# Performance work log

Measured on AMD Instinct MI355X. Metric: run time of the kernel, lower is better.

## Reference

```python
import jax, jax.numpy as jnp
import numpy as np

B, N, F_IN, H = 16, 1024, 64, 256
NEG = -9e15
ALPHA = 0.2  # LeakyReLU slope


def _leaky(x):
    return jnp.where(x >= 0, x, ALPHA * x)


def setup_inputs() -> dict:
    key = jax.random.key(0)
    ks = jax.random.split(key, 12)
    s = lambda k, shape, fan: jax.random.normal(k, shape, jnp.float32) / np.sqrt(fan)
    node_features = jax.random.normal(ks[0], (B, N, F_IN), jnp.float32)
    adj_matrix = jax.random.randint(ks[1], (B, N, N), 0, 2).astype(jnp.float32)
    return {
        "node_features": node_features,
        "adj_matrix": adj_matrix,
        "emb_W": s(ks[2], (F_IN, H), F_IN),
        "emb_b": jnp.zeros((H,), jnp.float32),
        "W0": s(ks[3], (H, H), H),
        "a1_0": s(ks[4], (H,), H),
        "a2_0": s(ks[5], (H,), H),
        "W1": s(ks[6], (H, H), H),
        "a1_1": s(ks[7], (H,), H),
        "a2_1": s(ks[8], (H,), H),
        "gp_W1": s(ks[9], (H, H), H),
        "gp_b1": jnp.zeros((H,), jnp.float32),
        "gp_W2": s(ks[10], (H, H), H),
        "gp_b2": jnp.zeros((H,), jnp.float32),
    }


def _gat_layer(x, mask, W, a1, a2):
    # x: [B,N,H]; mask: [B,N,N] bool. Equivalent to original concat trick:
    # a([h_i || h_j]) = h_i @ a1 + h_j @ a2 with a.weight split in halves.
    h = jnp.einsum('bnf,fo->bno', x, W)              # [B,N,H]
    s1 = jnp.einsum('bnh,h->bn', h, a1)              # [B,N]
    s2 = jnp.einsum('bnh,h->bn', h, a2)              # [B,N]
    e = _leaky(s1[:, :, None] + s2[:, None, :])      # [B,N,N]
    att = jax.nn.softmax(jnp.where(mask, e, NEG), axis=2)
    # dropout p=0.2 is identity in eval mode
    return jnp.einsum('bij,bjh->bih', att, h)        # [B,N,H]


def reference(node_features, adj_matrix, emb_W, emb_b,
              W0, a1_0, a2_0, W1, a1_1, a2_1,
              gp_W1, gp_b1, gp_W2, gp_b2):
    mask = adj_matrix > 0
    x = jnp.einsum('bnf,fh->bnh', node_features, emb_W) + emb_b
    x = jax.nn.relu(_gat_layer(x, mask, W0, a1_0, a2_0))
    x = jax.nn.relu(_gat_layer(x, mask, W1, a1_1, a2_1))
    g = jnp.mean(x, axis=1) + jnp.max(x, axis=1)     # [B,H]
    g = jax.nn.relu(g @ gp_W1 + gp_b1) @ gp_W2 + gp_b2
    return x, g
```

## Files before the change

### kernel.cpp

```cpp
#include <hip/hip_runtime.h>
#include <hip/hip_bf16.h>

#define B 16
#define N 1024
#define F_IN 64
#define H 256
#define ALPHA 0.2f
#define LOG2E 1.44269504f

typedef __attribute__((ext_vector_type(8))) _Float16 half8;
typedef __attribute__((ext_vector_type(4))) _Float16 half4;
typedef __attribute__((ext_vector_type(4))) float floatx4;
typedef __attribute__((ext_vector_type(16))) float floatx16;

#if __has_builtin(__builtin_amdgcn_exp2f)
#define EXP2F(x) __builtin_amdgcn_exp2f(x)
#else
#define EXP2F(x) exp2f(x)
#endif

__device__ __forceinline__ floatx4 mfma_f16(half8 a, half8 b, floatx4 c) {
    return __builtin_amdgcn_mfma_f32_16x16x32_f16(a, b, c, 0, 0, 0);
}
__device__ __forceinline__ floatx16 mfma32_f16(half8 a, half8 b, floatx16 c) {
    return __builtin_amdgcn_mfma_f32_32x32x16_f16(a, b, c, 0, 0, 0);
}

__global__ __launch_bounds__(256) void k_prep(const float* __restrict__ embW,
                                              const float* __restrict__ W0, const float* __restrict__ W1,
                                              const float* __restrict__ a10, const float* __restrict__ a20,
                                              const float* __restrict__ a11, const float* __restrict__ a21,
                                              _Float16* __restrict__ wBf,
                                              _Float16* __restrict__ embf,
                                              float* __restrict__ wa1, float* __restrict__ wa2,
                                              int* __restrict__ cnt) {
    __shared__ float lds[256 * 17];
    const int blk = blockIdx.x;
    const int t = threadIdx.x;
    const int lane = t & 63;

    if (blk == 34) {
        if (t < B) cnt[t] = 0;
        for (int s = t; s < 2048; s += 256) {
            const int ln = s & 63, ct2 = s >> 6;
            const int ct = ct2 >> 1, ks2 = ct2 & 1;
            const int q = ln >> 4, lw = ln & 15;
            half8 bf;
#pragma unroll
            for (int e = 0; e < 8; e++)
                bf[e] = (_Float16)embW[(ks2 * 32 + q * 8 + e) * H + ct * 16 + lw];
            *(half8*)(embf + (size_t)s * 8) = bf;
        }
        return;
    }
    if (blk >= 32) {
        const int l = blk - 32;
        const float* W = l ? W1 : W0;
        const float* a1 = l ? a11 : a10;
        const float* a2 = l ? a21 : a20;
        float* a1s = lds;
        float* a2s = lds + 256;
        a1s[t] = a1[t]; a2s[t] = a2[t];
        __syncthreads();
        float v1 = 0.f, v2 = 0.f;
        for (int c = 0; c < H; c += 4) {
            float4 w = *(const float4*)&W[t * H + c];
            v1 += w.x * a1s[c] + w.y * a1s[c + 1] + w.z * a1s[c + 2] + w.w * a1s[c + 3];
            v2 += w.x * a2s[c] + w.y * a2s[c + 1] + w.z * a2s[c + 2] + w.w * a2s[c + 3];
        }
        wa1[l * H + t] = v1;
        wa2[l * H + t] = v2;
        return;
    }
    const int l = blk >> 4, ct = blk & 15;
    const float* W = l ? W1 : W0;
#pragma unroll
    for (int rep = 0; rep < 16; rep++) {
        int idx = rep * 256 + t;
        int k = idx >> 4, cl = idx & 15;
        lds[k * 17 + cl] = W[k * H + ct * 16 + cl];
    }
    __syncthreads();
    const int w = t >> 6;
    const int l15 = lane & 15, quad = lane >> 4;
#pragma unroll
    for (int e = 0; e < 2; e++) {
        const int ks = w * 2 + e;
        half8 bf;
#pragma unroll
        for (int jj = 0; jj < 8; jj++)
            bf[jj] = (_Float16)lds[(ks * 32 + quad * 8 + jj) * 17 + l15];
        *(half8*)(wBf + (size_t)(((l * 16 + ct) * 8 + ks) * 64 + lane) * 8) = bf;
    }
}

#define XS(it, ks) ((((it) * 8 + (ks))) * 520)
__global__ __launch_bounds__(256, 4) void k_mix(const float* __restrict__ adj,
                                                const float* __restrict__ nf,
                                                const _Float16* __restrict__ embf,
                                                const float* __restrict__ embB,
                                                const _Float16* __restrict__ wBf,
                                                const float* __restrict__ wa1, const float* __restrict__ wa2,
                                                unsigned* __restrict__ mask32,
                                                _Float16* __restrict__ hB,
                                                float* __restrict__ s1, float* __restrict__ s2) {
    __shared__ __align__(16) _Float16 sm[8320];
    const int blk = blockIdx.x;
    const int t = threadIdx.x;
    const int lane = t & 63;

    if (blk & 1) {
        const int id = blk >> 1;
        const int wv = id * 4 + (t >> 6);
#pragma unroll 2
        for (int task = wv; task < B * N * 4; task += 4096) {
            const float4 v = *(const float4*)(adj + (size_t)task * 256 + lane * 4);
            unsigned long long b0 = __ballot(v.x > 0.f);
            unsigned long long b1 = __ballot(v.y > 0.f);
            unsigned long long b2 = __ballot(v.z > 0.f);
            unsigned long long b3 = __ballot(v.w > 0.f);
            if (lane < 8) {
                unsigned w0 = (unsigned)((b0 >> (8 * lane)) & 0xff)
                            | ((unsigned)((b1 >> (8 * lane)) & 0xff) << 8)
                            | ((unsigned)((b2 >> (8 * lane)) & 0xff) << 16)
                            | ((unsigned)((b3 >> (8 * lane)) & 0xff) << 24);
                const int jg = task & 3, row = task >> 2;
                mask32[(size_t)row * 32 + jg * 8 + lane] = w0;
            }
        }
        return;
    }

    const int lin = blk >> 1;
    const int rc = lin >> 1, chalf = lin & 1;
    const int row0 = rc * 32;
    const int w = t >> 6;
    const int l15 = lane & 15, quad = lane >> 4;

    {
        half8 anf[2][2];
#pragma unroll
        for (int it = 0; it < 2; it++)
#pragma unroll
            for (int ks2 = 0; ks2 < 2; ks2++) {
                const float* src = nf + (size_t)(row0 + it * 16 + l15) * F_IN + ks2 * 32 + quad * 8;
                float4 f0 = *(const float4*)(src);
                float4 f1 = *(const float4*)(src + 4);
                half8 a;
                a[0] = (_Float16)f0.x; a[1] = (_Float16)f0.y;
                a[2] = (_Float16)f0.z; a[3] = (_Float16)f0.w;
                a[4] = (_Float16)f1.x; a[5] = (_Float16)f1.y;
                a[6] = (_Float16)f1.z; a[7] = (_Float16)f1.w;
                anf[it][ks2] = a;
            }
#pragma unroll
        for (int ctl = 0; ctl < 4; ctl++) {
            const int ct = w * 4 + ctl;
            half8 be0 = *(const half8*)(embf + (size_t)((ct * 2 + 0) * 64 + lane) * 8);
            half8 be1 = *(const half8*)(embf + (size_t)((ct * 2 + 1) * 64 + lane) * 8);
            const int col = ct * 16 + l15;
            const float bias = embB[col];
            const int ks = col >> 5, qd = (col >> 3) & 3, e = col & 7;
#pragma unroll
            for (int it = 0; it < 2; it++) {
                floatx4 xa = {0.f, 0.f, 0.f, 0.f};
                xa = mfma_f16(anf[it][0], be0, xa);
                xa = mfma_f16(anf[it][1], be1, xa);
#pragma unroll
                for (int r = 0; r < 4; r++)
                    sm[XS(it, ks) + (qd * 16 + quad * 4 + r) * 8 + e] = (_Float16)(xa[r] + bias);
            }
        }
    }
    __syncthreads();

    const int ct0 = chalf * 8 + 2 * w;
    const _Float16* pB0 = wBf + (size_t)((ct0 * 8) * 64 + lane) * 8;
    const _Float16* pB1 = wBf + (size_t)(((ct0 + 1) * 8) * 64 + lane) * 8;

    floatx4 acc[2][2];
    floatx4 z = {0.f, 0.f, 0.f, 0.f};
    acc[0][0] = z; acc[0][1] = z; acc[1][0] = z; acc[1][1] = z;
    float sp1a = 0.f, sp2a = 0.f, sp1b = 0.f, sp2b = 0.f;

    half8 B0 = *(const half8*)(pB0);
    half8 B1 = *(const half8*)(pB1);

#pragma unroll
    for (int ks = 0; ks < 8; ks++) {
        half8 nB0 = B0, nB1 = B1;
        if (ks < 7) {
            const int o = (ks + 1) * 512;
            nB0 = *(const half8*)(pB0 + o);
            nB1 = *(const half8*)(pB1 + o);
        }
        half8 A0 = *(const half8*)(sm + XS(0, ks) + lane * 8);
        half8 A1 = *(const half8*)(sm + XS(1, ks) + lane * 8);
        acc[0][0] = mfma_f16(A0, B0, acc[0][0]);
        acc[0][1] = mfma_f16(A0, B1, acc[0][1]);
        acc[1][0] = mfma_f16(A1, B0, acc[1][0]);
        acc[1][1] = mfma_f16(A1, B1, acc[1][1]);
        if (chalf == 0 && w == 0) {
            float4 w1a = *(const float4*)(wa1 + ks * 32 + quad * 8);
            float4 w1b = *(const float4*)(wa1 + ks * 32 + quad * 8 + 4);
            float4 w2a = *(const float4*)(wa2 + ks * 32 + quad * 8);
            float4 w2b = *(const float4*)(wa2 + ks * 32 + quad * 8 + 4);
            float wv1[8] = {w1a.x, w1a.y, w1a.z, w1a.w, w1b.x, w1b.y, w1b.z, w1b.w};
            float wv2[8] = {w2a.x, w2a.y, w2a.z, w2a.w, w2b.x, w2b.y, w2b.z, w2b.w};
#pragma unroll
            for (int j = 0; j < 8; j++) {
                float xa = (float)A0[j];
                float xb = (float)A1[j];
                sp1a += xa * wv1[j]; sp2a += xa * wv2[j];
                sp1b += xb * wv1[j]; sp2b += xb * wv2[j];
            }
        }
        B0 = nB0; B1 = nB1;
    }

    __syncthreads();
    _Float16* trc = sm;
#pragma unroll
    for (int rg = 0; rg < 2; rg++) {
#pragma unroll
        for (int n2 = 0; n2 < 2; n2++) {
            const int c_l = (2 * w + n2) * 16 + l15;
            half4 hv;
            hv[0] = (_Float16)acc[rg][n2][0];
            hv[1] = (_Float16)acc[rg][n2][1];
            hv[2] = (_Float16)acc[rg][n2][2];
            hv[3] = (_Float16)acc[rg][n2][3];
            *(half4*)(trc + c_l * 40 + rg * 16 + quad * 4) = hv;
        }
    }
    __syncthreads();
    {
        const int bb = row0 >> 10, jtb = (row0 >> 5) & 31;
#pragma unroll
        for (int rep = 0; rep < 2; rep++) {
            int slot = rep * 256 + t;
            int l = slot & 63, frag = slot >> 6;
            int k4 = frag >> 1, ks = frag & 1;
            int c_l = k4 * 32 + (l & 31);
            int roff = ks * 16 + (l >> 5) * 8;
            half8 hv = *(const half8*)(trc + c_l * 40 + roff);
            _Float16* dst = hB + ((size_t)((bb * 8 + chalf * 4 + k4) * 32 + jtb) * 2 + ks) * 512 + l * 8;
            *(half8*)dst = hv;
        }
    }
    if (chalf == 0 && w == 0) {
        sp1a += __shfl_xor(sp1a, 16); sp1a += __shfl_xor(sp1a, 32);
        sp2a += __shfl_xor(sp2a, 16); sp2a += __shfl_xor(sp2a, 32);
        sp1b += __shfl_xor(sp1b, 16); sp1b += __shfl_xor(sp1b, 32);
        sp2b += __shfl_xor(sp2b, 16); sp2b += __shfl_xor(sp2b, 32);
        if (quad == 0) {
            s1[row0 + l15] = sp1a; s2[row0 + l15] = sp2a;
            s1[row0 + 16 + l15] = sp1b; s2[row0 + 16 + l15] = sp2b;
        }
    }
}

__global__ __launch_bounds__(256, 4) void k_gemm(const _Float16* __restrict__ xf,
                                                 const _Float16* __restrict__ wBf,
                                                 const float* __restrict__ wa1, const float* __restrict__ wa2,
                                                 _Float16* __restrict__ hB,
                                                 float* __restrict__ s1, float* __restrict__ s2) {
    __shared__ __align__(16) _Float16 sm[8320];
    const int lin = blockIdx.x;
    const int rc = lin >> 1, chalf = lin & 1;
    const int row0 = rc * 32;
    const int t = threadIdx.x;
    const int lane = t & 63, w = t >> 6;
    const int l15 = lane & 15, quad = lane >> 4;

#pragma unroll
    for (int pass = 0; pass < 4; pass++) {
        int idx = pass * 256 + t;
        int row_l = idx >> 5, k8 = idx & 31;
        half8 v = *(const half8*)(xf + (size_t)(row0 + row_l) * H + k8 * 8);
        int it = row_l >> 4, lf = row_l & 15, ks = k8 >> 2, qd = k8 & 3;
        *(half8*)(sm + XS(it, ks) + (qd * 16 + lf) * 8) = v;
    }
    __syncthreads();

    const int ct0 = chalf * 8 + 2 * w;
    const _Float16* pB0 = wBf + (size_t)((ct0 * 8) * 64 + lane) * 8;
    const _Float16* pB1 = wBf + (size_t)(((ct0 + 1) * 8) * 64 + lane) * 8;

    floatx4 acc[2][2];
    floatx4 z = {0.f, 0.f, 0.f, 0.f};
    acc[0][0] = z; acc[0][1] = z; acc[1][0] = z; acc[1][1] = z;
    float sp1a = 0.f, sp2a = 0.f, sp1b = 0.f, sp2b = 0.f;

    half8 B0 = *(const half8*)(pB0);
    half8 B1 = *(const half8*)(pB1);

#pragma unroll
    for (int ks = 0; ks < 8; ks++) {
        half8 nB0 = B0, nB1 = B1;
        if (ks < 7) {
            const int o = (ks + 1) * 512;
            nB0 = *(const half8*)(pB0 + o);
            nB1 = *(const half8*)(pB1 + o);
        }
        half8 A0 = *(const half8*)(sm + XS(0, ks) + lane * 8);
        half8 A1 = *(const half8*)(sm + XS(1, ks) + lane * 8);
        acc[0][0] = mfma_f16(A0, B0, acc[0][0]);
        acc[0][1] = mfma_f16(A0, B1, acc[0][1]);
        acc[1][0] = mfma_f16(A1, B0, acc[1][0]);
        acc[1][1] = mfma_f16(A1, B1, acc[1][1]);
        if (chalf == 0 && w == 0) {
            float4 w1a = *(const float4*)(wa1 + ks * 32 + quad * 8);
            float4 w1b = *(const float4*)(wa1 + ks * 32 + quad * 8 + 4);
            float4 w2a = *(const float4*)(wa2 + ks * 32 + quad * 8);
            float4 w2b = *(const float4*)(wa2 + ks * 32 + quad * 8 + 4);
            float wv1[8] = {w1a.x, w1a.y, w1a.z, w1a.w, w1b.x, w1b.y, w1b.z, w1b.w};
            float wv2[8] = {w2a.x, w2a.y, w2a.z, w2a.w, w2b.x, w2b.y, w2b.z, w2b.w};
#pragma unroll
            for (int j = 0; j < 8; j++) {
                float xa = (float)A0[j];
                float xb = (float)A1[j];
                sp1a += xa * wv1[j]; sp2a += xa * wv2[j];
                sp1b += xb * wv1[j]; sp2b += xb * wv2[j];
            }
        }
        B0 = nB0; B1 = nB1;
    }

    __syncthreads();
    _Float16* trc = sm;
#pragma unroll
    for (int rg = 0; rg < 2; rg++) {
#pragma unroll
        for (int n2 = 0; n2 < 2; n2++) {
            const int c_l = (2 * w + n2) * 16 + l15;
            half4 hv;
            hv[0] = (_Float16)acc[rg][n2][0];
            hv[1] = (_Float16)acc[rg][n2][1];
            hv[2] = (_Float16)acc[rg][n2][2];
            hv[3] = (_Float16)acc[rg][n2][3];
            *(half4*)(trc + c_l * 40 + rg * 16 + quad * 4) = hv;
        }
    }
    __syncthreads();
    {
        const int bb = row0 >> 10, jtb = (row0 >> 5) & 31;
#pragma unroll
        for (int rep = 0; rep < 2; rep++) {
            int slot = rep * 256 + t;
            int l = slot & 63, frag = slot >> 6;
            int k4 = frag >> 1, ks = frag & 1;
            int c_l = k4 * 32 + (l & 31);
            int roff = ks * 16 + (l >> 5) * 8;
            half8 hv = *(const half8*)(trc + c_l * 40 + roff);
            _Float16* dst = hB + ((size_t)((bb * 8 + chalf * 4 + k4) * 32 + jtb) * 2 + ks) * 512 + l * 8;
            *(half8*)dst = hv;
        }
    }
    if (chalf == 0 && w == 0) {
        sp1a += __shfl_xor(sp1a, 16); sp1a += __shfl_xor(sp1a, 32);
        sp2a += __shfl_xor(sp2a, 16); sp2a += __shfl_xor(sp2a, 32);
        sp1b += __shfl_xor(sp1b, 16); sp1b += __shfl_xor(sp1b, 32);
        sp2b += __shfl_xor(sp2b, 16); sp2b += __shfl_xor(sp2b, 32);
        if (quad == 0) {
            s1[row0 + l15] = sp1a; s2[row0 + l15] = sp2a;
            s1[row0 + 16 + l15] = sp1b; s2[row0 + 16 + l15] = sp2b;
        }
    }
}

template <int LAST>
__global__ __launch_bounds__(256, 1) void k_gat(const _Float16* __restrict__ hB,
                                                const float* __restrict__ s1g,
                                                const float* __restrict__ s2g,
                                                const unsigned* __restrict__ mask32,
                                                float* __restrict__ outf,
                                                _Float16* __restrict__ oxf,
                                                float* __restrict__ psum, float* __restrict__ pmax,
                                                const float* __restrict__ gpW1, const float* __restrict__ gpb1,
                                                const float* __restrict__ gpW2, const float* __restrict__ gpb2,
                                                float* __restrict__ gout, int* __restrict__ cnt) {
    __shared__ float s2s[N];
    __shared__ unsigned msk[128][33];
    __shared__ float wmax[4];
    __shared__ float red1[4][128];
    __shared__ float red2[4][128];
    __shared__ int lastf;
    const int lin = blockIdx.x;
    const int xcd = lin & 7, sl = lin >> 3;
    const int b = xcd * 2 + (sl & 1);
    const int chunk = (sl >> 1) & 7;
    const int chalf = sl >> 4;
    const int i0 = chunk * 128;
    const int t = threadIdx.x;
    const int lane = t & 63, w = t >> 6;
    const int l31 = lane & 31, hi = lane >> 5;
    const int hi2 = hi * 2, hi8 = hi * 8;

    float tm = -INFINITY;
    for (int idx = t; idx < N; idx += 256) {
        float v = s2g[b * N + idx] * LOG2E;
        s2s[idx] = v;
        tm = fmaxf(tm, v);
    }
#pragma unroll
    for (int off = 1; off <= 32; off <<= 1) tm = fmaxf(tm, __shfl_xor(tm, off));
    if (lane == 0) wmax[w] = tm;
#pragma unroll
    for (int pass = 0; pass < 16; pass++) {
        int idx = pass * 256 + t;
        int r = idx >> 5, wd = idx & 31;
        msk[r][wd] = mask32[(size_t)(b * N + i0 + r) * 32 + wd];
    }
    __syncthreads();
    const float s2maxL = fmaxf(fmaxf(wmax[0], wmax[1]), fmaxf(wmax[2], wmax[3]));

    const float s1L = s1g[b * N + i0 + w * 32 + l31] * LOG2E;
    const float tmx = s1L + s2maxL;
    const float mL = fmaxf(tmx, ALPHA * tmx);
    const float a1c = s1L - mL;
    const float a2c = fmaf(ALPHA, s1L, -mL);

    const _Float16* pb[4][2];
#pragma unroll
    for (int k4 = 0; k4 < 4; k4++)
#pragma unroll
        for (int ks = 0; ks < 2; ks++)
            pb[k4][ks] = hB + ((size_t)(b * 8 + chalf * 4 + k4) * 64 + ks) * 512 + lane * 8;

    floatx16 acc[4];
    floatx16 accl;
#pragma unroll
    for (int r = 0; r < 16; r++) accl[r] = 0.f;
#pragma unroll
    for (int k4 = 0; k4 < 4; k4++) acc[k4] = accl;

    half8 ones;
#pragma unroll
    for (int jj = 0; jj < 8; jj++) ones[jj] = (_Float16)1.0f;

    const float* svp = s2s + hi8;
    const unsigned* mr = &msk[w * 32 + l31][0];

    half8 bufA[4][2], bufB[4][2];
#pragma unroll
    for (int k4 = 0; k4 < 4; k4++) {
        bufA[k4][0] = *(const half8*)(pb[k4][0]);
        bufA[k4][1] = *(const half8*)(pb[k4][1]);
    }

#define GAT_STEP(JT, BUF)                                                      \
    do {                                                                       \
        const unsigned m = mr[JT];                                             \
        float4 sa0 = *(const float4*)(svp + (JT) * 32);                        \
        float4 sb0 = *(const float4*)(svp + (JT) * 32 + 4);                    \
        float4 sa1 = *(const float4*)(svp + (JT) * 32 + 16);                   \
        float4 sb1 = *(const float4*)(svp + (JT) * 32 + 20);                   \
        float sv0[8] = {sa0.x, sa0.y, sa0.z, sa0.w, sb0.x, sb0.y, sb0.z, sb0.w};\
        float sv1[8] = {sa1.x, sa1.y, sa1.z, sa1.w, sb1.x, sb1.y, sb1.z, sb1.w};\
        unsigned mq0 = m >> hi2;                                               \
        unsigned mq1 = m >> (4 + hi2);                                         \
        union { _Float16 h[8]; half8 v; } pk0, pk1;                            \
        _Pragma("unroll")                                                      \
        for (int e = 0; e < 8; e++) {                                          \
            const int bp = (e & 3) * 8 + (e >> 2);                             \
            float u0 = a1c + sv0[e];                                           \
            float v0 = fmaf(ALPHA, sv0[e], a2c);                               \
            float w0 = fmaxf(u0, v0);                                          \
            w0 = ((mq0 >> bp) & 1u) ? w0 : -126.f;                             \
            pk0.h[e] = (_Float16)EXP2F(w0);                                    \
            float u1 = a1c + sv1[e];                                           \
            float v1 = fmaf(ALPHA, sv1[e], a2c);                               \
            float w1 = fmaxf(u1, v1);                                          \
            w1 = ((mq1 >> bp) & 1u) ? w1 : -126.f;                             \
            pk1.h[e] = (_Float16)EXP2F(w1);                                    \
        }                                                                      \
        accl = mfma32_f16(pk0.v, ones, accl);                                  \
        _Pragma("unroll")                                                      \
        for (int k4 = 0; k4 < 4; k4++) acc[k4] = mfma32_f16(pk0.v, BUF[k4][0], acc[k4]); \
        accl = mfma32_f16(pk1.v, ones, accl);                                  \
        _Pragma("unroll")                                                      \
        for (int k4 = 0; k4 < 4; k4++) acc[k4] = mfma32_f16(pk1.v, BUF[k4][1], acc[k4]); \
    } while (0)

    for (int jt = 0; jt < 32; jt += 2) {
        {
            const int o = (jt + 1) * 1024;
#pragma unroll
            for (int k4 = 0; k4 < 4; k4++) {
                bufB[k4][0] = *(const half8*)(pb[k4][0] + o);
                bufB[k4][1] = *(const half8*)(pb[k4][1] + o);
            }
        }
        GAT_STEP(jt, bufA);
        if (jt + 2 < 32) {
            const int o = (jt + 2) * 1024;
#pragma unroll
            for (int k4 = 0; k4 < 4; k4++) {
                bufA[k4][0] = *(const half8*)(pb[k4][0] + o);
                bufA[k4][1] = *(const half8*)(pb[k4][1] + o);
            }
        }
        GAT_STEP(jt + 1, bufB);
    }
#undef GAT_STEP

    float invv[16];
#pragma unroll
    for (int r = 0; r < 16; r++) invv[r] = 1.f / accl[r];

    const size_t rowb = (size_t)b * N + i0 + w * 32 + 4 * hi;
    const int colbase = chalf * 128;
#pragma unroll
    for (int k4 = 0; k4 < 4; k4++) {
        const int c = colbase + k4 * 32 + l31;
        float cs = 0.f, cm = -INFINITY;
#pragma unroll
        for (int reg = 0; reg < 16; reg++) {
            const int roff = (reg & 3) + 8 * (reg >> 2);
            float v = fmaxf(acc[k4][reg] * invv[reg], 0.f);
            if (LAST) {
                outf[(rowb + roff) * H + c] = v;
                cs += v; cm = fmaxf(cm, v);
            } else {
                oxf[(rowb + roff) * H + c] = (_Float16)v;
            }
        }
        if (LAST) {
            cs += __shfl_xor(cs, 32);
            cm = fmaxf(cm, __shfl_xor(cm, 32));
            if (hi == 0) { red1[w][k4 * 32 + l31] = cs; red2[w][k4 * 32 + l31] = cm; }
        }
    }
    if (LAST) {
        __syncthreads();
        if (t < 128) {
            float s = red1[0][t] + red1[1][t] + red1[2][t] + red1[3][t];
            float m = fmaxf(fmaxf(red2[0][t], red2[1][t]), fmaxf(red2[2][t], red2[3][t]));
            __hip_atomic_store(&psum[(b * 8 + chunk) * H + chalf * 128 + t], s,
                               __ATOMIC_RELAXED, __HIP_MEMORY_SCOPE_AGENT);
            __hip_atomic_store(&pmax[(b * 8 + chunk) * H + chalf * 128 + t], m,
                               __ATOMIC_RELAXED, __HIP_MEMORY_SCOPE_AGENT);
        }
        asm volatile("s_waitcnt vmcnt(0)" ::: "memory");
        __syncthreads();
        if (t == 0) {
            int old = atomicAdd(&cnt[b], 1);
            lastf = (old == 15) ? 1 : 0;
        }
        __syncthreads();
        if (lastf) {
            float* g_s = s2s;
            float* t_s = s2s + 256;
            const int c = t;
            float s = 0.f, m = -INFINITY;
#pragma unroll
            for (int ch = 0; ch < 8; ch++) {
                s += __hip_atomic_load(&psum[(b * 8 + ch) * H + c],
                                       __ATOMIC_RELAXED, __HIP_MEMORY_SCOPE_AGENT);
                m = fmaxf(m, __hip_atomic_load(&pmax[(b * 8 + ch) * H + c],
                                               __ATOMIC_RELAXED, __HIP_MEMORY_SCOPE_AGENT));
            }
            g_s[c] = s * (1.f / N) + m;
            __syncthreads();
            float a = gpb1[c];
#pragma unroll 16
            for (int k = 0; k < H; k++) a += g_s[k] * gpW1[k * H + c];
            t_s[c] = fmaxf(a, 0.f);
            __syncthreads();
            float o = gpb2[c];
#pragma unroll 16
            for (int k = 0; k < H; k++) o += t_s[k] * gpW2[k * H + c];
            gout[b * H + c] = o;
        }
    }
}

extern "C" void kernel_launch(void* const* d_in, const int* in_sizes, int n_in,
                              void* d_out, int out_size, void* d_ws, size_t ws_size,
                              hipStream_t stream) {
    const float* nf    = (const float*)d_in[0];
    const float* adj   = (const float*)d_in[1];
    const float* emb_W = (const float*)d_in[2];
    const float* emb_b = (const float*)d_in[3];
    const float* W0    = (const float*)d_in[4];
    const float* a1_0  = (const float*)d_in[5];
    const float* a2_0  = (const float*)d_in[6];
    const float* W1    = (const float*)d_in[7];
    const float* a1_1  = (const float*)d_in[8];
    const float* a2_1  = (const float*)d_in[9];
    const float* gpW1  = (const float*)d_in[10];
    const float* gpb1  = (const float*)d_in[11];
    const float* gpW2  = (const float*)d_in[12];
    const float* gpb2  = (const float*)d_in[13];

    float* xout = (float*)d_out;
    float* gout = xout + B * N * H;

    char* w = (char*)d_ws;
    _Float16* xf     = (_Float16*)(w);
    _Float16* hB     = (_Float16*)(w + 8388608);
    unsigned* mask32 = (unsigned*)(w + 16777216);
    float* s1        = (float*)(w + 18874368);
    float* s2        = (float*)(w + 18939904);
    _Float16* wBf    = (_Float16*)(w + 19005440);
    float* wa1       = (float*)(w + 19267584);
    float* wa2       = (float*)(w + 19269632);
    float* psum      = (float*)(w + 19271680);
    float* pmax      = (float*)(w + 19533824);
    _Float16* embf   = (_Float16*)(w + 19795968);
    int* cnt         = (int*)(w + 19828736);

    k_prep<<<35, 256, 0, stream>>>(emb_W, W0, W1, a1_0, a2_0, a1_1, a2_1,
                                   wBf, embf, wa1, wa2, cnt);

    k_mix<<<2048, 256, 0, stream>>>(adj, nf, embf, emb_b, wBf, wa1, wa2,
                                    mask32, hB, s1, s2);
    k_gat<0><<<256, 256, 0, stream>>>(hB, s1, s2, mask32, nullptr, xf,
                                      nullptr, nullptr, nullptr, nullptr,
                                      nullptr, nullptr, nullptr, nullptr);

    k_gemm<<<1024, 256, 0, stream>>>(xf, wBf + 65536, wa1 + H, wa2 + H, hB, s1, s2);
    k_gat<1><<<256, 256, 0, stream>>>(hB, s1, s2, mask32, xout, nullptr,
                                      psum, pmax, gpW1, gpb1, gpW2, gpb2,
                                      gout, cnt);
}
```

Before: 222.9 us.

## Split GAT attention kernel into 64-column quarters to double block count

Each k_gat block now covers 64 output columns instead of 128, so the grid doubles to 512 blocks and launch bounds allow two blocks per CU. The aim is better CU occupancy and latency hiding on a GPU with many CUs, where 256 blocks left units idle. The cost is that every block recomputes the exp/softmax weights for its rows, so that work is duplicated four times per row instead of twice. The completion counter threshold for the final pooling reduction is raised to match the extra blocks.

```diff
diff --git a/kernel.cpp b/kernel.cpp
--- a/kernel.cpp
+++ b/kernel.cpp
@@ -370,7 +370,7 @@
 }
 
 template <int LAST>
-__global__ __launch_bounds__(256, 1) void k_gat(const _Float16* __restrict__ hB,
+__global__ __launch_bounds__(256, 2) void k_gat(const _Float16* __restrict__ hB,
                                                 const float* __restrict__ s1g,
                                                 const float* __restrict__ s2g,
                                                 const unsigned* __restrict__ mask32,
@@ -383,14 +383,15 @@
     __shared__ float s2s[N];
     __shared__ unsigned msk[128][33];
     __shared__ float wmax[4];
-    __shared__ float red1[4][128];
-    __shared__ float red2[4][128];
+    __shared__ float red1[4][64];
+    __shared__ float red2[4][64];
     __shared__ int lastf;
     const int lin = blockIdx.x;
     const int xcd = lin & 7, sl = lin >> 3;
     const int b = xcd * 2 + (sl & 1);
     const int chunk = (sl >> 1) & 7;
-    const int chalf = sl >> 4;
+    const int colq = sl >> 4;
+    const int ctb = colq * 2;
     const int i0 = chunk * 128;
     const int t = threadIdx.x;
     const int lane = t & 63, w = t >> 6;
@@ -421,19 +422,18 @@
     const float a1c = s1L - mL;
     const float a2c = fmaf(ALPHA, s1L, -mL);
 
-    const _Float16* pb[4][2];
-#pragma unroll
-    for (int k4 = 0; k4 < 4; k4++)
+    const _Float16* pb[2][2];
+#pragma unroll
+    for (int k2 = 0; k2 < 2; k2++)
 #pragma unroll
         for (int ks = 0; ks < 2; ks++)
-            pb[k4][ks] = hB + ((size_t)(b * 8 + chalf * 4 + k4) * 64 + ks) * 512 + lane * 8;
-
-    floatx16 acc[4];
+            pb[k2][ks] = hB + ((size_t)(b * 8 + ctb + k2) * 64 + ks) * 512 + lane * 8;
+
+    floatx16 acc[2];
     floatx16 accl;
 #pragma unroll
     for (int r = 0; r < 16; r++) accl[r] = 0.f;
-#pragma unroll
-    for (int k4 = 0; k4 < 4; k4++) acc[k4] = accl;
+    acc[0] = accl; acc[1] = accl;
 
     half8 ones;
 #pragma unroll
@@ -442,11 +442,11 @@
     const float* svp = s2s + hi8;
     const unsigned* mr = &msk[w * 32 + l31][0];
 
-    half8 bufA[4][2], bufB[4][2];
-#pragma unroll
-    for (int k4 = 0; k4 < 4; k4++) {
-        bufA[k4][0] = *(const half8*)(pb[k4][0]);
-        bufA[k4][1] = *(const half8*)(pb[k4][1]);
+    half8 bufA[2][2], bufB[2][2];
+#pragma unroll
+    for (int k2 = 0; k2 < 2; k2++) {
+        bufA[k2][0] = *(const half8*)(pb[k2][0]);
+        bufA[k2][1] = *(const half8*)(pb[k2][1]);
     }
 
 #define GAT_STEP(JT, BUF)                                                      \
@@ -476,29 +476,29 @@
             pk1.h[e] = (_Float16)EXP2F(w1);                                    \
         }                                                                      \
         accl = mfma32_f16(pk0.v, ones, accl);                                  \
-        _Pragma("unroll")                                                      \
-        for (int k4 = 0; k4 < 4; k4++) acc[k4] = mfma32_f16(pk0.v, BUF[k4][0], acc[k4]); \
+        acc[0] = mfma32_f16(pk0.v, BUF[0][0], acc[0]);                         \
+        acc[1] = mfma32_f16(pk0.v, BUF[1][0], acc[1]);                         \
         accl = mfma32_f16(pk1.v, ones, accl);                                  \
-        _Pragma("unroll")                                                      \
-        for (int k4 = 0; k4 < 4; k4++) acc[k4] = mfma32_f16(pk1.v, BUF[k4][1], acc[k4]); \
+        acc[0] = mfma32_f16(pk1.v, BUF[0][1], acc[0]);                         \
+        acc[1] = mfma32_f16(pk1.v, BUF[1][1], acc[1]);                         \
     } while (0)
 
     for (int jt = 0; jt < 32; jt += 2) {
         {
             const int o = (jt + 1) * 1024;
 #pragma unroll
-            for (int k4 = 0; k4 < 4; k4++) {
-                bufB[k4][0] = *(const half8*)(pb[k4][0] + o);
-                bufB[k4][1] = *(const half8*)(pb[k4][1] + o);
+            for (int k2 = 0; k2 < 2; k2++) {
+                bufB[k2][0] = *(const half8*)(pb[k2][0] + o);
+                bufB[k2][1] = *(const half8*)(pb[k2][1] + o);
             }
         }
         GAT_STEP(jt, bufA);
         if (jt + 2 < 32) {
             const int o = (jt + 2) * 1024;
 #pragma unroll
-            for (int k4 = 0; k4 < 4; k4++) {
-                bufA[k4][0] = *(const half8*)(pb[k4][0] + o);
-                bufA[k4][1] = *(const half8*)(pb[k4][1] + o);
+            for (int k2 = 0; k2 < 2; k2++) {
+                bufA[k2][0] = *(const half8*)(pb[k2][0] + o);
+                bufA[k2][1] = *(const half8*)(pb[k2][1] + o);
             }
         }
         GAT_STEP(jt + 1, bufB);
@@ -510,15 +510,14 @@
     for (int r = 0; r < 16; r++) invv[r] = 1.f / accl[r];
 
     const size_t rowb = (size_t)b * N + i0 + w * 32 + 4 * hi;
-    const int colbase = chalf * 128;
-#pragma unroll
-    for (int k4 = 0; k4 < 4; k4++) {
-        const int c = colbase + k4 * 32 + l31;
+#pragma unroll
+    for (int k2 = 0; k2 < 2; k2++) {
+        const int c = colq * 64 + k2 * 32 + l31;
         float cs = 0.f, cm = -INFINITY;
 #pragma unroll
         for (int reg = 0; reg < 16; reg++) {
             const int roff = (reg & 3) + 8 * (reg >> 2);
-            float v = fmaxf(acc[k4][reg] * invv[reg], 0.f);
+            float v = fmaxf(acc[k2][reg] * invv[reg], 0.f);
             if (LAST) {
                 outf[(rowb + roff) * H + c] = v;
                 cs += v; cm = fmaxf(cm, v);
@@ -529,24 +528,24 @@
         if (LAST) {
             cs += __shfl_xor(cs, 32);
             cm = fmaxf(cm, __shfl_xor(cm, 32));
-            if (hi == 0) { red1[w][k4 * 32 + l31] = cs; red2[w][k4 * 32 + l31] = cm; }
+            if (hi == 0) { red1[w][k2 * 32 + l31] = cs; red2[w][k2 * 32 + l31] = cm; }
         }
     }
     if (LAST) {
         __syncthreads();
-        if (t < 128) {
+        if (t < 64) {
             float s = red1[0][t] + red1[1][t] + red1[2][t] + red1[3][t];
             float m = fmaxf(fmaxf(red2[0][t], red2[1][t]), fmaxf(red2[2][t], red2[3][t]));
-            __hip_atomic_store(&psum[(b * 8 + chunk) * H + chalf * 128 + t], s,
+            __hip_atomic_store(&psum[(b * 8 + chunk) * H + colq * 64 + t], s,
                                __ATOMIC_RELAXED, __HIP_MEMORY_SCOPE_AGENT);
-            __hip_atomic_store(&pmax[(b * 8 + chunk) * H + chalf * 128 + t], m,
+            __hip_atomic_store(&pmax[(b * 8 + chunk) * H + colq * 64 + t], m,
                                __ATOMIC_RELAXED, __HIP_MEMORY_SCOPE_AGENT);
         }
         asm volatile("s_waitcnt vmcnt(0)" ::: "memory");
         __syncthreads();
         if (t == 0) {
             int old = atomicAdd(&cnt[b], 1);
-            lastf = (old == 15) ? 1 : 0;
+            lastf = (old == 31) ? 1 : 0;
         }
         __syncthreads();
         if (lastf) {
@@ -616,12 +615,12 @@
 
     k_mix<<<2048, 256, 0, stream>>>(adj, nf, embf, emb_b, wBf, wa1, wa2,
                                     mask32, hB, s1, s2);
-    k_gat<0><<<256, 256, 0, stream>>>(hB, s1, s2, mask32, nullptr, xf,
+    k_gat<0><<<512, 256, 0, stream>>>(hB, s1, s2, mask32, nullptr, xf,
                                       nullptr, nullptr, nullptr, nullptr,
                                       nullptr, nullptr, nullptr, nullptr);
 
     k_gemm<<<1024, 256, 0, stream>>>(xf, wBf + 65536, wa1 + H, wa2 + H, hB, s1, s2);
-    k_gat<1><<<256, 256, 0, stream>>>(hB, s1, s2, mask32, xout, nullptr,
+    k_gat<1><<<512, 256, 0, stream>>>(hB, s1, s2, mask32, xout, nullptr,
                                       psum, pmax, gpW1, gpb1, gpW2, gpb2,
                                       gout, cnt);
 }
```

New measurement: 225.8 us. About the same (+1.3%).
